# Kernel optimization log

Measured on AMD Instinct MI355X. Metric: run time of the kernel, lower is better.

Reference implementation:

```python
import jax, jax.numpy as jnp
import numpy as np

NUM_TASKS = 5
POOL = 5
R = 8
TOPK = 3
SCALE = 1.0  # module self.scale and forward scale arg, both 1
B, S, DIN, DOUT = 4, 4096, 1024, 1024


def setup_inputs() -> dict:
    key = jax.random.key(0)
    ks = jax.random.split(key, 5)
    inp = {
        "input": jax.random.normal(ks[0], (B, S, DIN), dtype=jnp.float32),
        "W": jax.random.normal(ks[1], (DOUT, DIN), dtype=jnp.float32) / np.sqrt(DIN),
        "lora_down": jax.random.normal(ks[2], (POOL, DIN, R), dtype=jnp.float32) / np.sqrt(DIN),
        "lora_up": jax.random.normal(ks[3], (POOL, R, DOUT), dtype=jnp.float32) / np.sqrt(R),
        "lora_route": jax.random.normal(ks[4], (NUM_TASKS, DIN, POOL), dtype=jnp.float32) * 0.02,
        "task_id": 4,
    }
    return inp


def reference(input, W, lora_down, lora_up, lora_route, task_id):
    # Eval branch (self.training == False), 1 <= task_id <= num_tasks.
    task_id = min(task_id, NUM_TASKS)
    k = min(task_id, TOPK)
    route = lora_route[1]                          # [DIN, POOL] (detach split is a no-op for fwd)
    input_mean = jnp.mean(input, axis=1)           # [B, DIN]
    lora_omegas = jnp.mean(input_mean @ route, axis=0)  # [POOL]
    sliced = lora_omegas[1:task_id + 1]            # source slices from 1
    G, I = jax.lax.top_k(sliced, k)                # indices used DIRECTLY (as in source)
    gate = jax.nn.softmax(G)                       # [k]
    # detached expert products (eval path detaches lora_down @ lora_up)
    dw = jax.lax.stop_gradient(
        jnp.einsum('kdr,kro->kdo', lora_down[I], lora_up[I]))  # [k, DIN, DOUT]
    # delta = sum_i gate[i] * SCALE * (input @ dw[i]); forward scale arg = 1
    delta = SCALE * jnp.einsum('k,bsd,kdo->bso', gate, input, dw)
    # delta_w_all[:B//2] = 0
    bmask = (jnp.arange(input.shape[0]) >= input.shape[0] // 2).astype(delta.dtype)
    delta = delta * bmask[:, None, None]
    return input @ W.T + delta
```

## Files before the change

### kernel.cpp

```cpp
#include <hip/hip_runtime.h>
#include <hip/hip_bf16.h>

typedef __attribute__((ext_vector_type(8))) __bf16 bf16x8;
typedef __attribute__((ext_vector_type(4))) __bf16 bf16x4;
typedef __attribute__((ext_vector_type(4))) float f32x4;

#define DIN 1024
#define DOUT 1024
#define BB 4
#define SS 4096
#define MROWS (BB*SS)
#define POOLN 5
#define RR 8
#define NTASKS 5
#define TOPKK 3

__global__ __launch_bounds__(256) void kA_colsum(const float* __restrict__ in,
                                                 float* __restrict__ partial) {
    const int t = threadIdx.x;
    const int b = blockIdx.x;
    const int tid = b * 256 + t;
    const f32x4* __restrict__ inv = (const f32x4*)in;

    float s0 = 0.f, s1 = 0.f, s2 = 0.f, s3 = 0.f;
    size_t ia = (size_t)tid;
    size_t ib = (size_t)tid + 2097152;
    f32x4 ca = inv[ia];
    f32x4 cb = inv[ib];
#pragma unroll
    for (int i = 0; i < 4; ++i) {
        f32x4 na = ca, nb = cb;
        if (i < 3) {
            na = inv[ia + 524288];
            nb = inv[ib + 524288];
        }
        s0 += ca[0] + cb[0]; s1 += ca[1] + cb[1];
        s2 += ca[2] + cb[2]; s3 += ca[3] + cb[3];
        ca = na; cb = nb;
        ia += 524288; ib += 524288;
    }
    const int c0 = (t * 4) & (DIN - 1);
    f32x4 p = { s0, s1, s2, s3 };
    *(f32x4*)&partial[(size_t)b * DIN + c0] = p;
}

__global__ __launch_bounds__(256) void k1b_reduce(const float* __restrict__ partial,
                                                  float* __restrict__ partial2) {
    const int tid = blockIdx.x * 256 + threadIdx.x;
    const int c = tid & (DIN - 1);
    const int g = tid >> 10;
    float s = 0.f;
    const int r0 = g * 256;
#pragma unroll 8
    for (int r = r0; r < r0 + 256; ++r)
        s += partial[(size_t)r * DIN + c];
    partial2[(size_t)g * DIN + c] = s;
}

__global__ __launch_bounds__(256) void k23_weights(const float* __restrict__ partial2,
                                                   const float* __restrict__ lroute,
                                                   const int* __restrict__ task_id_p,
                                                   const float* __restrict__ W,
                                                   const float* __restrict__ ldown,
                                                   const float* __restrict__ lup,
                                                   __bf16* __restrict__ Wb0,
                                                   __bf16* __restrict__ Wb1) {
    __shared__ float red[4][POOLN];
    __shared__ float sgate[TOPKK];
    __shared__ int   sgidx[TOPKK];
    const int tix = threadIdx.x;
    const int w = tix >> 6, l = tix & 63;

    float part[POOLN] = {0.f, 0.f, 0.f, 0.f, 0.f};
    {
        const int d0 = tix * 4;
#pragma unroll
        for (int dd = 0; dd < 4; ++dd) {
            const int d = d0 + dd;
            float cs = 0.f;
#pragma unroll
            for (int g = 0; g < 8; ++g) cs += partial2[g * DIN + d];
            cs *= (1.0f / (float)MROWS);
            const float* rp = &lroute[(size_t)1 * DIN * POOLN + (size_t)d * POOLN];
#pragma unroll
            for (int p = 0; p < POOLN; ++p) part[p] += cs * rp[p];
        }
    }
#pragma unroll
    for (int p = 0; p < POOLN; ++p) {
        float v = part[p];
        for (int off = 32; off; off >>= 1) v += __shfl_down(v, off);
        if (l == 0) red[w][p] = v;
    }
    __syncthreads();
    if (tix == 0) {
#pragma unroll
        for (int p = 0; p < POOLN; ++p)
            part[p] = red[0][p] + red[1][p] + red[2][p] + red[3][p];
        int tid = *task_id_p;
        if (tid > NTASKS) tid = NTASKS;
        int L = tid < (POOLN - 1) ? tid : (POOLN - 1);
        int k = tid < TOPKK ? tid : TOPKK;
        float sl[POOLN];
        for (int j = 0; j < L; ++j) sl[j] = part[1 + j];
        float G[TOPKK]; int I[TOPKK];
        int used = 0;
        for (int j = 0; j < k; ++j) {
            int best = -1; float bv = 0.f;
            for (int i2 = 0; i2 < L; ++i2) {
                if (used & (1 << i2)) continue;
                if (best < 0 || sl[i2] > bv) { bv = sl[i2]; best = i2; }
            }
            used |= 1 << best; G[j] = bv; I[j] = best;
        }
        float gt[TOPKK] = {0.f, 0.f, 0.f};
        int   gi[TOPKK] = {0, 0, 0};
        if (k > 0) {
            float m = G[0];
            float e[TOPKK]; float se = 0.f;
            for (int j = 0; j < k; ++j) { e[j] = expf(G[j] - m); se += e[j]; }
            for (int j = 0; j < k; ++j) { gt[j] = e[j] / se; gi[j] = I[j]; }
        }
#pragma unroll
        for (int j = 0; j < TOPKK; ++j) { sgate[j] = gt[j]; sgidx[j] = gi[j]; }
    }
    __syncthreads();

    const int o = blockIdx.x;
    const int t = tix;
    float c[TOPKK][RR];
#pragma unroll
    for (int j = 0; j < TOPKK; ++j) {
        const float g = sgate[j];
        const int   p = sgidx[j];
#pragma unroll
        for (int r = 0; r < RR; ++r)
            c[j][r] = g * lup[(size_t)p * RR * DOUT + (size_t)r * DOUT + o];
    }
    const int d0 = t * 4;
    const float4 wv = *(const float4*)&W[(size_t)o * DIN + d0];
    float outv[4] = { wv.x, wv.y, wv.z, wv.w };
    float dwv[4]  = { 0.f, 0.f, 0.f, 0.f };
#pragma unroll
    for (int j = 0; j < TOPKK; ++j) {
        const int p = sgidx[j];
#pragma unroll
        for (int dd = 0; dd < 4; ++dd) {
            const float4 da = *(const float4*)&ldown[(size_t)p * DIN * RR + (size_t)(d0 + dd) * RR];
            const float4 db = *(const float4*)&ldown[(size_t)p * DIN * RR + (size_t)(d0 + dd) * RR + 4];
            dwv[dd] += da.x * c[j][0] + da.y * c[j][1] + da.z * c[j][2] + da.w * c[j][3]
                     + db.x * c[j][4] + db.y * c[j][5] + db.z * c[j][6] + db.w * c[j][7];
        }
    }
    bf16x4 b0 = { (__bf16)outv[0], (__bf16)outv[1], (__bf16)outv[2], (__bf16)outv[3] };
    bf16x4 b1 = { (__bf16)(outv[0] + dwv[0]), (__bf16)(outv[1] + dwv[1]),
                  (__bf16)(outv[2] + dwv[2]), (__bf16)(outv[3] + dwv[3]) };
    *(bf16x4*)&Wb0[(size_t)o * DIN + d0] = b0;
    *(bf16x4*)&Wb1[(size_t)o * DIN + d0] = b1;
}

__global__ __launch_bounds__(512, 4) void k4_gemm(const float* __restrict__ A,
                                                  const __bf16* __restrict__ B0,
                                                  const __bf16* __restrict__ B1,
                                                  float* __restrict__ C) {
    __shared__ ushort lds[36864];
    const int bid = blockIdx.x;
    const int xcd = bid & 7;
    const int idx = bid >> 3;
    const int tm  = xcd * 16 + (idx >> 2);
    const int tn  = idx & 3;
    const __bf16* __restrict__ Bt = (tm >= 64) ? B1 : B0;

    const int tix  = threadIdx.x;
    const int lane = tix & 63;
    const int wid  = tix >> 6;
    const int wm = wid >> 2, wn = wid & 3;

    const int ar = tix >> 2;
    const int ac = tix & 3;
    const f32x4* __restrict__ pA = (const f32x4*)(A + ((size_t)(tm * 128 + ar)) * 1024 + ac * 8);
    const int awrp  = tix >> 3;
    const int awslot= ((tix & 3) + 4 * ((tix >> 2) & 1)) ^ (awrp & 7);
    const int awoff = awrp * 64 + awslot * 8;

    const int rpl  = lane >> 3;
    const int sl   = (lane & 7) ^ rpl;
    const int srow = rpl * 2 + (sl >> 2);
    const int sc   = sl & 3;
    const char* gB = (const char*)Bt + ((size_t)(tn*256 + wid*32 + srow)) * 2048 + sc * 16;
    const int ldsBst = 4096 + wid * 1024;

    const int rhalf = (lane & 15) >> 1;
    const int slot  = ((lane >> 4) + 4 * (lane & 1)) ^ rhalf;
    const int aoff  = (wm * 32 + rhalf) * 64 + slot * 8;
    const int boff  = 4096 + (wn * 32 + rhalf) * 64 + slot * 8;

    f32x4 acc[4][4];
#pragma unroll
    for (int i = 0; i < 4; ++i)
#pragma unroll
        for (int j = 0; j < 4; ++j) acc[i][j] = (f32x4){0.f, 0.f, 0.f, 0.f};

    auto issueB = [&](int s) {
        const int p = s % 3;
        const size_t kb = (size_t)s * 64;
#pragma unroll
        for (int j = 0; j < 2; ++j) {
            __builtin_amdgcn_global_load_lds(
                (const __attribute__((address_space(1))) void*)(gB + (size_t)j * 32768 + kb),
                (__attribute__((address_space(3))) void*)&lds[p * 12288 + ldsBst + j * 512],
                16, 0, 0);
        }
    };

    auto writeA = [&](int s, f32x4 a0, f32x4 a1) {
        const int p = s % 3;
        bf16x8 v = { (__bf16)a0[0], (__bf16)a0[1], (__bf16)a0[2], (__bf16)a0[3],
                     (__bf16)a1[0], (__bf16)a1[1], (__bf16)a1[2], (__bf16)a1[3] };
        *(bf16x8*)&lds[p * 12288 + awoff] = v;
    };

    auto computeSlab = [&](int s) {
        const int p = s % 3;
        const ushort* aB = &lds[p * 12288 + aoff];
        const ushort* bB = &lds[p * 12288 + boff];
        bf16x8 a[4], b[4];
#pragma unroll
        for (int mi = 0; mi < 4; ++mi) a[mi] = *(const bf16x8*)(aB + mi * 512);
#pragma unroll
        for (int ni = 0; ni < 4; ++ni) b[ni] = *(const bf16x8*)(bB + ni * 512);
        __builtin_amdgcn_s_setprio(1);
#pragma unroll
        for (int mi = 0; mi < 4; ++mi)
#pragma unroll
            for (int ni = 0; ni < 4; ++ni)
                acc[mi][ni] = __builtin_amdgcn_mfma_f32_16x16x32_bf16(
                    a[mi], b[ni], acc[mi][ni], 0, 0, 0);
        __builtin_amdgcn_s_setprio(0);
    };

    f32x4 pa0 = pA[0], pa1 = pA[1];
    issueB(0);
    f32x4 na0 = pA[8], na1 = pA[9];
    issueB(1);
    asm volatile("s_waitcnt vmcnt(6)" ::: "memory");
    writeA(0, pa0, pa1);
    asm volatile("s_waitcnt lgkmcnt(0)" ::: "memory");

#pragma unroll 1
    for (int s = 0; s < 32; ++s) {
        if (s < 31) {
            asm volatile("s_waitcnt vmcnt(2)" ::: "memory");
            writeA(s + 1, na0, na1);
        } else {
            asm volatile("s_waitcnt vmcnt(0)" ::: "memory");
        }
        if (s < 30) {
            na0 = pA[(size_t)(s + 2) * 8];
            na1 = pA[(size_t)(s + 2) * 8 + 1];
            issueB(s + 2);
        }
        __builtin_amdgcn_s_barrier();
        asm volatile("" ::: "memory");
        computeSlab(s);
        asm volatile("" ::: "memory");
        asm volatile("s_waitcnt lgkmcnt(0)" ::: "memory");
        __builtin_amdgcn_s_barrier();
    }

#pragma unroll
    for (int mi = 0; mi < 4; ++mi) {
#pragma unroll
        for (int r = 0; r < 4; ++r) {
            const int grow = tm * 128 + wm * 64 + mi * 16 + (lane >> 4) * 4 + r;
            float* cp = C + (size_t)grow * 1024 + tn * 256 + wn * 64 + (lane & 15);
#pragma unroll
            for (int ni = 0; ni < 4; ++ni) cp[ni * 16] = acc[mi][ni][r];
        }
    }
}

extern "C" void kernel_launch(void* const* d_in, const int* in_sizes, int n_in,
                              void* d_out, int out_size, void* d_ws, size_t ws_size,
                              hipStream_t stream) {
    const float* in     = (const float*)d_in[0];
    const float* W      = (const float*)d_in[1];
    const float* ldown  = (const float*)d_in[2];
    const float* lup    = (const float*)d_in[3];
    const float* lroute = (const float*)d_in[4];
    const int*   taskid = (const int*)d_in[5];
    float* out = (float*)d_out;

    __bf16* Wb0     = (__bf16*)d_ws;
    __bf16* Wb1     = Wb0 + (size_t)DOUT * DIN;
    float*  partial2= (float*)(Wb1 + (size_t)DOUT * DIN);
    float*  partial = partial2 + 8 * DIN + 64;

    kA_colsum<<<2048, 256, 0, stream>>>(in, partial);
    k1b_reduce<<<32, 256, 0, stream>>>(partial, partial2);
    k23_weights<<<1024, 256, 0, stream>>>(partial2, lroute, taskid, W, ldown, lup, Wb0, Wb1);
    k4_gemm<<<512, 512, 0, stream>>>(in, Wb0, Wb1, out);
}
```

Baseline: 94.83 us.

## Fuse colsum, reduce and weight-prep kernels into one grid-synced front kernel

Three preliminary kernels (column-sum partials, partial reduction, routing plus merged weight build) become one 512-block kernel. Each block first reduces its input slice and projects it onto the routing matrix, so only 5 floats per block are written instead of a 1024-wide partial row. The blocks then meet at a flag-based grid barrier before every block computes top-k and builds two output rows. This removes two kernel launches and the large partial buffers, at the cost of a memset launch and a spin-wait that needs all 512 blocks to be resident at once.

```diff
diff --git a/kernel.cpp b/kernel.cpp
--- a/kernel.cpp
+++ b/kernel.cpp
@@ -7,156 +7,153 @@
 
 #define DIN 1024
 #define DOUT 1024
-#define BB 4
-#define SS 4096
-#define MROWS (BB*SS)
+#define MROWS 16384
 #define POOLN 5
 #define RR 8
 #define NTASKS 5
 #define TOPKK 3
 
-__global__ __launch_bounds__(256) void kA_colsum(const float* __restrict__ in,
-                                                 float* __restrict__ partial) {
-    const int t = threadIdx.x;
-    const int b = blockIdx.x;
-    const int tid = b * 256 + t;
-    const f32x4* __restrict__ inv = (const f32x4*)in;
-
-    float s0 = 0.f, s1 = 0.f, s2 = 0.f, s3 = 0.f;
-    size_t ia = (size_t)tid;
-    size_t ib = (size_t)tid + 2097152;
-    f32x4 ca = inv[ia];
-    f32x4 cb = inv[ib];
-#pragma unroll
-    for (int i = 0; i < 4; ++i) {
-        f32x4 na = ca, nb = cb;
-        if (i < 3) {
-            na = inv[ia + 524288];
-            nb = inv[ib + 524288];
-        }
-        s0 += ca[0] + cb[0]; s1 += ca[1] + cb[1];
-        s2 += ca[2] + cb[2]; s3 += ca[3] + cb[3];
-        ca = na; cb = nb;
-        ia += 524288; ib += 524288;
-    }
-    const int c0 = (t * 4) & (DIN - 1);
-    f32x4 p = { s0, s1, s2, s3 };
-    *(f32x4*)&partial[(size_t)b * DIN + c0] = p;
-}
-
-__global__ __launch_bounds__(256) void k1b_reduce(const float* __restrict__ partial,
-                                                  float* __restrict__ partial2) {
-    const int tid = blockIdx.x * 256 + threadIdx.x;
-    const int c = tid & (DIN - 1);
-    const int g = tid >> 10;
-    float s = 0.f;
-    const int r0 = g * 256;
-#pragma unroll 8
-    for (int r = r0; r < r0 + 256; ++r)
-        s += partial[(size_t)r * DIN + c];
-    partial2[(size_t)g * DIN + c] = s;
-}
-
-__global__ __launch_bounds__(256) void k23_weights(const float* __restrict__ partial2,
-                                                   const float* __restrict__ lroute,
-                                                   const int* __restrict__ task_id_p,
-                                                   const float* __restrict__ W,
-                                                   const float* __restrict__ ldown,
-                                                   const float* __restrict__ lup,
-                                                   __bf16* __restrict__ Wb0,
-                                                   __bf16* __restrict__ Wb1) {
+__global__ __launch_bounds__(256, 4) void kFront(
+        const float* __restrict__ in, const float* __restrict__ W,
+        const float* __restrict__ ldown, const float* __restrict__ lup,
+        const float* __restrict__ lroute, const int* __restrict__ task_id_p,
+        __bf16* __restrict__ Wb0, __bf16* __restrict__ Wb1,
+        float* __restrict__ omgpart, unsigned* __restrict__ flags) {
     __shared__ float red[4][POOLN];
     __shared__ float sgate[TOPKK];
     __shared__ int   sgidx[TOPKK];
-    const int tix = threadIdx.x;
-    const int w = tix >> 6, l = tix & 63;
-
-    float part[POOLN] = {0.f, 0.f, 0.f, 0.f, 0.f};
+    const int b = blockIdx.x;
+    const int t = threadIdx.x;
+    const int w = t >> 6, l = t & 63;
+
+    const f32x4* __restrict__ inv = (const f32x4*)in;
+    float s0 = 0.f, s1 = 0.f, s2 = 0.f, s3 = 0.f;
+    size_t ia = (size_t)b * 32 * 256 + t;
+    size_t ib = ia + 16 * 256;
+    f32x4 ca = inv[ia], cb = inv[ib];
+#pragma unroll
+    for (int i = 0; i < 16; ++i) {
+        f32x4 na = ca, nb = cb;
+        if (i < 15) { na = inv[ia + 256]; nb = inv[ib + 256]; }
+        s0 += ca[0] + cb[0]; s1 += ca[1] + cb[1];
+        s2 += ca[2] + cb[2]; s3 += ca[3] + cb[3];
+        ca = na; cb = nb; ia += 256; ib += 256;
+    }
+
+    float om[POOLN];
     {
-        const int d0 = tix * 4;
-#pragma unroll
-        for (int dd = 0; dd < 4; ++dd) {
-            const int d = d0 + dd;
-            float cs = 0.f;
-#pragma unroll
-            for (int g = 0; g < 8; ++g) cs += partial2[g * DIN + d];
-            cs *= (1.0f / (float)MROWS);
-            const float* rp = &lroute[(size_t)1 * DIN * POOLN + (size_t)d * POOLN];
-#pragma unroll
-            for (int p = 0; p < POOLN; ++p) part[p] += cs * rp[p];
-        }
+        const float* rp = &lroute[(size_t)DIN * POOLN + (size_t)(4 * t) * POOLN];
+        const float sj[4] = { s0, s1, s2, s3 };
+#pragma unroll
+        for (int p = 0; p < POOLN; ++p) om[p] = 0.f;
+#pragma unroll
+        for (int j = 0; j < 4; ++j)
+#pragma unroll
+            for (int p = 0; p < POOLN; ++p)
+                om[p] += sj[j] * rp[j * POOLN + p];
     }
 #pragma unroll
     for (int p = 0; p < POOLN; ++p) {
-        float v = part[p];
+        float v = om[p];
         for (int off = 32; off; off >>= 1) v += __shfl_down(v, off);
         if (l == 0) red[w][p] = v;
     }
     __syncthreads();
-    if (tix == 0) {
+    if (t == 0) {
 #pragma unroll
         for (int p = 0; p < POOLN; ++p)
-            part[p] = red[0][p] + red[1][p] + red[2][p] + red[3][p];
-        int tid = *task_id_p;
-        if (tid > NTASKS) tid = NTASKS;
-        int L = tid < (POOLN - 1) ? tid : (POOLN - 1);
-        int k = tid < TOPKK ? tid : TOPKK;
-        float sl[POOLN];
-        for (int j = 0; j < L; ++j) sl[j] = part[1 + j];
-        float G[TOPKK]; int I[TOPKK];
-        int used = 0;
-        for (int j = 0; j < k; ++j) {
-            int best = -1; float bv = 0.f;
-            for (int i2 = 0; i2 < L; ++i2) {
-                if (used & (1 << i2)) continue;
-                if (best < 0 || sl[i2] > bv) { bv = sl[i2]; best = i2; }
+            omgpart[b * 8 + p] = red[0][p] + red[1][p] + red[2][p] + red[3][p];
+        __threadfence();
+        __hip_atomic_store(&flags[b], 1u, __ATOMIC_RELEASE, __HIP_MEMORY_SCOPE_AGENT);
+    }
+
+    while (__hip_atomic_load(&flags[t], __ATOMIC_RELAXED, __HIP_MEMORY_SCOPE_AGENT) == 0u)
+        __builtin_amdgcn_s_sleep(8);
+    while (__hip_atomic_load(&flags[t + 256], __ATOMIC_RELAXED, __HIP_MEMORY_SCOPE_AGENT) == 0u)
+        __builtin_amdgcn_s_sleep(8);
+    __syncthreads();
+    __threadfence();
+
+    {
+        float acc[POOLN];
+#pragma unroll
+        for (int p = 0; p < POOLN; ++p)
+            acc[p] = omgpart[t * 8 + p] + omgpart[(t + 256) * 8 + p];
+#pragma unroll
+        for (int p = 0; p < POOLN; ++p) {
+            float v = acc[p];
+            for (int off = 32; off; off >>= 1) v += __shfl_down(v, off);
+            if (l == 0) red[w][p] = v;
+        }
+        __syncthreads();
+        if (t == 0) {
+            float part[POOLN];
+#pragma unroll
+            for (int p = 0; p < POOLN; ++p)
+                part[p] = (red[0][p] + red[1][p] + red[2][p] + red[3][p]) * (1.0f / (float)MROWS);
+            int tid = *task_id_p;
+            if (tid > NTASKS) tid = NTASKS;
+            int L = tid < (POOLN - 1) ? tid : (POOLN - 1);
+            int k = tid < TOPKK ? tid : TOPKK;
+            float sl[POOLN];
+            for (int j = 0; j < L; ++j) sl[j] = part[1 + j];
+            float G[TOPKK]; int I[TOPKK];
+            int used = 0;
+            for (int j = 0; j < k; ++j) {
+                int best = -1; float bv = 0.f;
+                for (int i2 = 0; i2 < L; ++i2) {
+                    if (used & (1 << i2)) continue;
+                    if (best < 0 || sl[i2] > bv) { bv = sl[i2]; best = i2; }
+                }
+                used |= 1 << best; G[j] = bv; I[j] = best;
             }
-            used |= 1 << best; G[j] = bv; I[j] = best;
-        }
-        float gt[TOPKK] = {0.f, 0.f, 0.f};
-        int   gi[TOPKK] = {0, 0, 0};
-        if (k > 0) {
-            float m = G[0];
-            float e[TOPKK]; float se = 0.f;
-            for (int j = 0; j < k; ++j) { e[j] = expf(G[j] - m); se += e[j]; }
-            for (int j = 0; j < k; ++j) { gt[j] = e[j] / se; gi[j] = I[j]; }
-        }
-#pragma unroll
-        for (int j = 0; j < TOPKK; ++j) { sgate[j] = gt[j]; sgidx[j] = gi[j]; }
-    }
-    __syncthreads();
-
-    const int o = blockIdx.x;
-    const int t = tix;
-    float c[TOPKK][RR];
-#pragma unroll
-    for (int j = 0; j < TOPKK; ++j) {
-        const float g = sgate[j];
-        const int   p = sgidx[j];
-#pragma unroll
-        for (int r = 0; r < RR; ++r)
-            c[j][r] = g * lup[(size_t)p * RR * DOUT + (size_t)r * DOUT + o];
-    }
-    const int d0 = t * 4;
-    const float4 wv = *(const float4*)&W[(size_t)o * DIN + d0];
-    float outv[4] = { wv.x, wv.y, wv.z, wv.w };
-    float dwv[4]  = { 0.f, 0.f, 0.f, 0.f };
-#pragma unroll
-    for (int j = 0; j < TOPKK; ++j) {
-        const int p = sgidx[j];
-#pragma unroll
-        for (int dd = 0; dd < 4; ++dd) {
-            const float4 da = *(const float4*)&ldown[(size_t)p * DIN * RR + (size_t)(d0 + dd) * RR];
-            const float4 db = *(const float4*)&ldown[(size_t)p * DIN * RR + (size_t)(d0 + dd) * RR + 4];
-            dwv[dd] += da.x * c[j][0] + da.y * c[j][1] + da.z * c[j][2] + da.w * c[j][3]
-                     + db.x * c[j][4] + db.y * c[j][5] + db.z * c[j][6] + db.w * c[j][7];
-        }
-    }
-    bf16x4 b0 = { (__bf16)outv[0], (__bf16)outv[1], (__bf16)outv[2], (__bf16)outv[3] };
-    bf16x4 b1 = { (__bf16)(outv[0] + dwv[0]), (__bf16)(outv[1] + dwv[1]),
-                  (__bf16)(outv[2] + dwv[2]), (__bf16)(outv[3] + dwv[3]) };
-    *(bf16x4*)&Wb0[(size_t)o * DIN + d0] = b0;
-    *(bf16x4*)&Wb1[(size_t)o * DIN + d0] = b1;
+            float gt[TOPKK] = {0.f, 0.f, 0.f};
+            int   gi[TOPKK] = {0, 0, 0};
+            if (k > 0) {
+                float m = G[0];
+                float e[TOPKK]; float se = 0.f;
+                for (int j = 0; j < k; ++j) { e[j] = expf(G[j] - m); se += e[j]; }
+                for (int j = 0; j < k; ++j) { gt[j] = e[j] / se; gi[j] = I[j]; }
+            }
+#pragma unroll
+            for (int j = 0; j < TOPKK; ++j) { sgate[j] = gt[j]; sgidx[j] = gi[j]; }
+        }
+        __syncthreads();
+    }
+
+#pragma unroll
+    for (int rep = 0; rep < 2; ++rep) {
+        const int o = b * 2 + rep;
+        float c[TOPKK][RR];
+#pragma unroll
+        for (int j = 0; j < TOPKK; ++j) {
+            const float g = sgate[j];
+            const int   p = sgidx[j];
+#pragma unroll
+            for (int r = 0; r < RR; ++r)
+                c[j][r] = g * lup[(size_t)p * RR * DOUT + (size_t)r * DOUT + o];
+        }
+        const int d0 = t * 4;
+        const float4 wv = *(const float4*)&W[(size_t)o * DIN + d0];
+        float outv[4] = { wv.x, wv.y, wv.z, wv.w };
+        float dwv[4]  = { 0.f, 0.f, 0.f, 0.f };
+#pragma unroll
+        for (int j = 0; j < TOPKK; ++j) {
+            const int p = sgidx[j];
+#pragma unroll
+            for (int dd = 0; dd < 4; ++dd) {
+                const float4 da = *(const float4*)&ldown[(size_t)p * DIN * RR + (size_t)(d0 + dd) * RR];
+                const float4 db = *(const float4*)&ldown[(size_t)p * DIN * RR + (size_t)(d0 + dd) * RR + 4];
+                dwv[dd] += da.x * c[j][0] + da.y * c[j][1] + da.z * c[j][2] + da.w * c[j][3]
+                         + db.x * c[j][4] + db.y * c[j][5] + db.z * c[j][6] + db.w * c[j][7];
+            }
+        }
+        bf16x4 b0 = { (__bf16)outv[0], (__bf16)outv[1], (__bf16)outv[2], (__bf16)outv[3] };
+        bf16x4 b1 = { (__bf16)(outv[0] + dwv[0]), (__bf16)(outv[1] + dwv[1]),
+                      (__bf16)(outv[2] + dwv[2]), (__bf16)(outv[3] + dwv[3]) };
+        *(bf16x4*)&Wb0[(size_t)o * DIN + d0] = b0;
+        *(bf16x4*)&Wb1[(size_t)o * DIN + d0] = b1;
+    }
 }
 
 __global__ __launch_bounds__(512, 4) void k4_gemm(const float* __restrict__ A,
@@ -291,13 +288,13 @@
     const int*   taskid = (const int*)d_in[5];
     float* out = (float*)d_out;
 
-    __bf16* Wb0     = (__bf16*)d_ws;
-    __bf16* Wb1     = Wb0 + (size_t)DOUT * DIN;
-    float*  partial2= (float*)(Wb1 + (size_t)DOUT * DIN);
-    float*  partial = partial2 + 8 * DIN + 64;
-
-    kA_colsum<<<2048, 256, 0, stream>>>(in, partial);
-    k1b_reduce<<<32, 256, 0, stream>>>(partial, partial2);
-    k23_weights<<<1024, 256, 0, stream>>>(partial2, lroute, taskid, W, ldown, lup, Wb0, Wb1);
+    __bf16*   Wb0     = (__bf16*)d_ws;
+    __bf16*   Wb1     = Wb0 + (size_t)DOUT * DIN;
+    float*    omgpart = (float*)(Wb1 + (size_t)DOUT * DIN);
+    unsigned* flags   = (unsigned*)(omgpart + 512 * 8);
+
+    hipMemsetAsync(flags, 0, 512 * sizeof(unsigned), stream);
+    kFront<<<512, 256, 0, stream>>>(in, W, ldown, lup, lroute, taskid,
+                                    Wb0, Wb1, omgpart, flags);
     k4_gemm<<<512, 512, 0, stream>>>(in, Wb0, Wb1, out);
 }
```

After: 127.6 us. 34.5% more time.

## Overlap first-half GEMM with column-sum reduction in a mixed kernel

Applied to the files above, without the earlier changes.

Splits the GEMM so the batch half that needs only plain W (bf16 converted by a new small kernel) runs in the same launch as the input column-sum blocks. The route-dependent corrected weight is then built and the second half GEMM runs separately. The aim is to hide the input-mean reduction and weight prep behind useful GEMM work instead of serialising them before the whole GEMM. In exchange it adds a launch and splits the GEMM into two 256-block launches, which may underfill the GPU and leave tails.

```diff
diff --git a/kernel.cpp b/kernel.cpp
--- a/kernel.cpp
+++ b/kernel.cpp
@@ -7,41 +7,172 @@
 
 #define DIN 1024
 #define DOUT 1024
-#define BB 4
-#define SS 4096
-#define MROWS (BB*SS)
+#define MROWS 16384
 #define POOLN 5
 #define RR 8
 #define NTASKS 5
 #define TOPKK 3
 
-__global__ __launch_bounds__(256) void kA_colsum(const float* __restrict__ in,
+__device__ __forceinline__ void gemm_tile(const float* __restrict__ A,
+                                          const __bf16* __restrict__ Bt,
+                                          float* __restrict__ C,
+                                          int tm, int tn, int tix,
+                                          ushort* lds) {
+    const int lane = tix & 63;
+    const int wid  = tix >> 6;
+    const int wm = wid >> 2, wn = wid & 3;
+
+    const int ar = tix >> 2;
+    const int ac = tix & 3;
+    const f32x4* __restrict__ pA = (const f32x4*)(A + ((size_t)(tm * 128 + ar)) * 1024 + ac * 8);
+    const int awrp  = tix >> 3;
+    const int awslot= ((tix & 3) + 4 * ((tix >> 2) & 1)) ^ (awrp & 7);
+    const int awoff = awrp * 64 + awslot * 8;
+
+    const int rpl  = lane >> 3;
+    const int sl   = (lane & 7) ^ rpl;
+    const int srow = rpl * 2 + (sl >> 2);
+    const int sc   = sl & 3;
+    const char* gB = (const char*)Bt + ((size_t)(tn*256 + wid*32 + srow)) * 2048 + sc * 16;
+    const int ldsBst = 4096 + wid * 1024;
+
+    const int rhalf = (lane & 15) >> 1;
+    const int slot  = ((lane >> 4) + 4 * (lane & 1)) ^ rhalf;
+    const int aoff  = (wm * 32 + rhalf) * 64 + slot * 8;
+    const int boff  = 4096 + (wn * 32 + rhalf) * 64 + slot * 8;
+
+    f32x4 acc[4][4];
+#pragma unroll
+    for (int i = 0; i < 4; ++i)
+#pragma unroll
+        for (int j = 0; j < 4; ++j) acc[i][j] = (f32x4){0.f, 0.f, 0.f, 0.f};
+
+    auto issueB = [&](int s) {
+        const int p = s % 3;
+        const size_t kb = (size_t)s * 64;
+#pragma unroll
+        for (int j = 0; j < 2; ++j) {
+            __builtin_amdgcn_global_load_lds(
+                (const __attribute__((address_space(1))) void*)(gB + (size_t)j * 32768 + kb),
+                (__attribute__((address_space(3))) void*)&lds[p * 12288 + ldsBst + j * 512],
+                16, 0, 0);
+        }
+    };
+
+    auto writeA = [&](int s, f32x4 a0, f32x4 a1) {
+        const int p = s % 3;
+        bf16x8 v = { (__bf16)a0[0], (__bf16)a0[1], (__bf16)a0[2], (__bf16)a0[3],
+                     (__bf16)a1[0], (__bf16)a1[1], (__bf16)a1[2], (__bf16)a1[3] };
+        *(bf16x8*)&lds[p * 12288 + awoff] = v;
+    };
+
+    auto computeSlab = [&](int s) {
+        const int p = s % 3;
+        const ushort* aB = &lds[p * 12288 + aoff];
+        const ushort* bB = &lds[p * 12288 + boff];
+        bf16x8 a[4], b[4];
+#pragma unroll
+        for (int mi = 0; mi < 4; ++mi) a[mi] = *(const bf16x8*)(aB + mi * 512);
+#pragma unroll
+        for (int ni = 0; ni < 4; ++ni) b[ni] = *(const bf16x8*)(bB + ni * 512);
+        __builtin_amdgcn_s_setprio(1);
+#pragma unroll
+        for (int mi = 0; mi < 4; ++mi)
+#pragma unroll
+            for (int ni = 0; ni < 4; ++ni)
+                acc[mi][ni] = __builtin_amdgcn_mfma_f32_16x16x32_bf16(
+                    a[mi], b[ni], acc[mi][ni], 0, 0, 0);
+        __builtin_amdgcn_s_setprio(0);
+    };
+
+    f32x4 pa0 = pA[0], pa1 = pA[1];
+    issueB(0);
+    f32x4 na0 = pA[8], na1 = pA[9];
+    issueB(1);
+    asm volatile("s_waitcnt vmcnt(6)" ::: "memory");
+    writeA(0, pa0, pa1);
+    asm volatile("s_waitcnt lgkmcnt(0)" ::: "memory");
+
+#pragma unroll 1
+    for (int s = 0; s < 32; ++s) {
+        if (s < 31) {
+            asm volatile("s_waitcnt vmcnt(2)" ::: "memory");
+            writeA(s + 1, na0, na1);
+        } else {
+            asm volatile("s_waitcnt vmcnt(0)" ::: "memory");
+        }
+        if (s < 30) {
+            na0 = pA[(size_t)(s + 2) * 8];
+            na1 = pA[(size_t)(s + 2) * 8 + 1];
+            issueB(s + 2);
+        }
+        __builtin_amdgcn_s_barrier();
+        asm volatile("" ::: "memory");
+        computeSlab(s);
+        asm volatile("" ::: "memory");
+        asm volatile("s_waitcnt lgkmcnt(0)" ::: "memory");
+        __builtin_amdgcn_s_barrier();
+    }
+
+#pragma unroll
+    for (int mi = 0; mi < 4; ++mi) {
+#pragma unroll
+        for (int r = 0; r < 4; ++r) {
+            const int grow = tm * 128 + wm * 64 + mi * 16 + (lane >> 4) * 4 + r;
+            float* cp = C + (size_t)grow * 1024 + tn * 256 + wn * 64 + (lane & 15);
+#pragma unroll
+            for (int ni = 0; ni < 4; ++ni) cp[ni * 16] = acc[mi][ni][r];
+        }
+    }
+}
+
+__global__ __launch_bounds__(256) void kW_cvt(const float* __restrict__ W,
+                                              __bf16* __restrict__ Wb0) {
+    const size_t i = (size_t)(blockIdx.x * 256 + threadIdx.x) * 8;
+    f32x4 a = *(const f32x4*)&W[i];
+    f32x4 b = *(const f32x4*)&W[i + 4];
+    bf16x8 v = { (__bf16)a[0], (__bf16)a[1], (__bf16)a[2], (__bf16)a[3],
+                 (__bf16)b[0], (__bf16)b[1], (__bf16)b[2], (__bf16)b[3] };
+    *(bf16x8*)&Wb0[i] = v;
+}
+
+__global__ __launch_bounds__(512, 4) void k1_mix(const float* __restrict__ in,
+                                                 const __bf16* __restrict__ Wb0,
+                                                 float* __restrict__ C,
                                                  float* __restrict__ partial) {
-    const int t = threadIdx.x;
-    const int b = blockIdx.x;
-    const int tid = b * 256 + t;
-    const f32x4* __restrict__ inv = (const f32x4*)in;
-
+    __shared__ ushort lds[36864];
+    const int bid = blockIdx.x;
+    if (bid < 256) {
+        const int xcd = bid & 7;
+        const int idx = bid >> 3;
+        gemm_tile(in, Wb0, C, xcd * 8 + (idx >> 2), idx & 3, threadIdx.x, lds);
+        return;
+    }
+    const int cb = bid - 256;
+    const int t  = threadIdx.x;
+    const int cq = t & 255;
+    const int h  = t >> 8;
+    const f32x4* __restrict__ base = (const f32x4*)in
+        + ((size_t)(cb * 256 + h * 128)) * 256 + cq;
     float s0 = 0.f, s1 = 0.f, s2 = 0.f, s3 = 0.f;
-    size_t ia = (size_t)tid;
-    size_t ib = (size_t)tid + 2097152;
-    f32x4 ca = inv[ia];
-    f32x4 cb = inv[ib];
-#pragma unroll
-    for (int i = 0; i < 4; ++i) {
-        f32x4 na = ca, nb = cb;
-        if (i < 3) {
-            na = inv[ia + 524288];
-            nb = inv[ib + 524288];
-        }
-        s0 += ca[0] + cb[0]; s1 += ca[1] + cb[1];
-        s2 += ca[2] + cb[2]; s3 += ca[3] + cb[3];
-        ca = na; cb = nb;
-        ia += 524288; ib += 524288;
-    }
-    const int c0 = (t * 4) & (DIN - 1);
-    f32x4 p = { s0, s1, s2, s3 };
-    *(f32x4*)&partial[(size_t)b * DIN + c0] = p;
+#pragma unroll 1
+    for (int j = 0; j < 16; ++j) {
+        const f32x4* p = base + (size_t)j * 8 * 256;
+        f32x4 v0 = p[0];
+        f32x4 v1 = p[256];
+        f32x4 v2 = p[512];
+        f32x4 v3 = p[768];
+        f32x4 v4 = p[1024];
+        f32x4 v5 = p[1280];
+        f32x4 v6 = p[1536];
+        f32x4 v7 = p[1792];
+        s0 += v0[0] + v1[0] + v2[0] + v3[0] + v4[0] + v5[0] + v6[0] + v7[0];
+        s1 += v0[1] + v1[1] + v2[1] + v3[1] + v4[1] + v5[1] + v6[1] + v7[1];
+        s2 += v0[2] + v1[2] + v2[2] + v3[2] + v4[2] + v5[2] + v6[2] + v7[2];
+        s3 += v0[3] + v1[3] + v2[3] + v3[3] + v4[3] + v5[3] + v6[3] + v7[3];
+    }
+    f32x4 pv = { s0, s1, s2, s3 };
+    *(f32x4*)&partial[(size_t)(cb * 2 + h) * DIN + cq * 4] = pv;
 }
 
 __global__ __launch_bounds__(256) void k1b_reduce(const float* __restrict__ partial,
@@ -50,21 +181,20 @@
     const int c = tid & (DIN - 1);
     const int g = tid >> 10;
     float s = 0.f;
-    const int r0 = g * 256;
+    const int r0 = g * 16;
 #pragma unroll 8
-    for (int r = r0; r < r0 + 256; ++r)
+    for (int r = r0; r < r0 + 16; ++r)
         s += partial[(size_t)r * DIN + c];
     partial2[(size_t)g * DIN + c] = s;
 }
 
-__global__ __launch_bounds__(256) void k23_weights(const float* __restrict__ partial2,
-                                                   const float* __restrict__ lroute,
-                                                   const int* __restrict__ task_id_p,
-                                                   const float* __restrict__ W,
-                                                   const float* __restrict__ ldown,
-                                                   const float* __restrict__ lup,
-                                                   __bf16* __restrict__ Wb0,
-                                                   __bf16* __restrict__ Wb1) {
+__global__ __launch_bounds__(256) void k23b_weights(const float* __restrict__ partial2,
+                                                    const float* __restrict__ lroute,
+                                                    const int* __restrict__ task_id_p,
+                                                    const float* __restrict__ W,
+                                                    const float* __restrict__ ldown,
+                                                    const float* __restrict__ lup,
+                                                    __bf16* __restrict__ Wb1) {
     __shared__ float red[4][POOLN];
     __shared__ float sgate[TOPKK];
     __shared__ int   sgidx[TOPKK];
@@ -127,7 +257,6 @@
     __syncthreads();
 
     const int o = blockIdx.x;
-    const int t = tix;
     float c[TOPKK][RR];
 #pragma unroll
     for (int j = 0; j < TOPKK; ++j) {
@@ -137,10 +266,9 @@
         for (int r = 0; r < RR; ++r)
             c[j][r] = g * lup[(size_t)p * RR * DOUT + (size_t)r * DOUT + o];
     }
-    const int d0 = t * 4;
+    const int d0 = tix * 4;
     const float4 wv = *(const float4*)&W[(size_t)o * DIN + d0];
-    float outv[4] = { wv.x, wv.y, wv.z, wv.w };
-    float dwv[4]  = { 0.f, 0.f, 0.f, 0.f };
+    float dwv[4] = { 0.f, 0.f, 0.f, 0.f };
 #pragma unroll
     for (int j = 0; j < TOPKK; ++j) {
         const int p = sgidx[j];
@@ -152,132 +280,19 @@
                      + db.x * c[j][4] + db.y * c[j][5] + db.z * c[j][6] + db.w * c[j][7];
         }
     }
-    bf16x4 b0 = { (__bf16)outv[0], (__bf16)outv[1], (__bf16)outv[2], (__bf16)outv[3] };
-    bf16x4 b1 = { (__bf16)(outv[0] + dwv[0]), (__bf16)(outv[1] + dwv[1]),
-                  (__bf16)(outv[2] + dwv[2]), (__bf16)(outv[3] + dwv[3]) };
-    *(bf16x4*)&Wb0[(size_t)o * DIN + d0] = b0;
+    bf16x4 b1 = { (__bf16)(wv.x + dwv[0]), (__bf16)(wv.y + dwv[1]),
+                  (__bf16)(wv.z + dwv[2]), (__bf16)(wv.w + dwv[3]) };
     *(bf16x4*)&Wb1[(size_t)o * DIN + d0] = b1;
 }
 
-__global__ __launch_bounds__(512, 4) void k4_gemm(const float* __restrict__ A,
-                                                  const __bf16* __restrict__ B0,
-                                                  const __bf16* __restrict__ B1,
+__global__ __launch_bounds__(512, 4) void k3_gemm(const float* __restrict__ in,
+                                                  const __bf16* __restrict__ Wb1,
                                                   float* __restrict__ C) {
     __shared__ ushort lds[36864];
     const int bid = blockIdx.x;
     const int xcd = bid & 7;
     const int idx = bid >> 3;
-    const int tm  = xcd * 16 + (idx >> 2);
-    const int tn  = idx & 3;
-    const __bf16* __restrict__ Bt = (tm >= 64) ? B1 : B0;
-
-    const int tix  = threadIdx.x;
-    const int lane = tix & 63;
-    const int wid  = tix >> 6;
-    const int wm = wid >> 2, wn = wid & 3;
-
-    const int ar = tix >> 2;
-    const int ac = tix & 3;
-    const f32x4* __restrict__ pA = (const f32x4*)(A + ((size_t)(tm * 128 + ar)) * 1024 + ac * 8);
-    const int awrp  = tix >> 3;
-    const int awslot= ((tix & 3) + 4 * ((tix >> 2) & 1)) ^ (awrp & 7);
-    const int awoff = awrp * 64 + awslot * 8;
-
-    const int rpl  = lane >> 3;
-    const int sl   = (lane & 7) ^ rpl;
-    const int srow = rpl * 2 + (sl >> 2);
-    const int sc   = sl & 3;
-    const char* gB = (const char*)Bt + ((size_t)(tn*256 + wid*32 + srow)) * 2048 + sc * 16;
-    const int ldsBst = 4096 + wid * 1024;
-
-    const int rhalf = (lane & 15) >> 1;
-    const int slot  = ((lane >> 4) + 4 * (lane & 1)) ^ rhalf;
-    const int aoff  = (wm * 32 + rhalf) * 64 + slot * 8;
-    const int boff  = 4096 + (wn * 32 + rhalf) * 64 + slot * 8;
-
-    f32x4 acc[4][4];
-#pragma unroll
-    for (int i = 0; i < 4; ++i)
-#pragma unroll
-        for (int j = 0; j < 4; ++j) acc[i][j] = (f32x4){0.f, 0.f, 0.f, 0.f};
-
-    auto issueB = [&](int s) {
-        const int p = s % 3;
-        const size_t kb = (size_t)s * 64;
-#pragma unroll
-        for (int j = 0; j < 2; ++j) {
-            __builtin_amdgcn_global_load_lds(
-                (const __attribute__((address_space(1))) void*)(gB + (size_t)j * 32768 + kb),
-                (__attribute__((address_space(3))) void*)&lds[p * 12288 + ldsBst + j * 512],
-                16, 0, 0);
-        }
-    };
-
-    auto writeA = [&](int s, f32x4 a0, f32x4 a1) {
-        const int p = s % 3;
-        bf16x8 v = { (__bf16)a0[0], (__bf16)a0[1], (__bf16)a0[2], (__bf16)a0[3],
-                     (__bf16)a1[0], (__bf16)a1[1], (__bf16)a1[2], (__bf16)a1[3] };
-        *(bf16x8*)&lds[p * 12288 + awoff] = v;
-    };
-
-    auto computeSlab = [&](int s) {
-        const int p = s % 3;
-        const ushort* aB = &lds[p * 12288 + aoff];
-        const ushort* bB = &lds[p * 12288 + boff];
-        bf16x8 a[4], b[4];
-#pragma unroll
-        for (int mi = 0; mi < 4; ++mi) a[mi] = *(const bf16x8*)(aB + mi * 512);
-#pragma unroll
-        for (int ni = 0; ni < 4; ++ni) b[ni] = *(const bf16x8*)(bB + ni * 512);
-        __builtin_amdgcn_s_setprio(1);
-#pragma unroll
-        for (int mi = 0; mi < 4; ++mi)
-#pragma unroll
-            for (int ni = 0; ni < 4; ++ni)
-                acc[mi][ni] = __builtin_amdgcn_mfma_f32_16x16x32_bf16(
-                    a[mi], b[ni], acc[mi][ni], 0, 0, 0);
-        __builtin_amdgcn_s_setprio(0);
-    };
-
-    f32x4 pa0 = pA[0], pa1 = pA[1];
-    issueB(0);
-    f32x4 na0 = pA[8], na1 = pA[9];
-    issueB(1);
-    asm volatile("s_waitcnt vmcnt(6)" ::: "memory");
-    writeA(0, pa0, pa1);
-    asm volatile("s_waitcnt lgkmcnt(0)" ::: "memory");
-
-#pragma unroll 1
-    for (int s = 0; s < 32; ++s) {
-        if (s < 31) {
-            asm volatile("s_waitcnt vmcnt(2)" ::: "memory");
-            writeA(s + 1, na0, na1);
-        } else {
-            asm volatile("s_waitcnt vmcnt(0)" ::: "memory");
-        }
-        if (s < 30) {
-            na0 = pA[(size_t)(s + 2) * 8];
-            na1 = pA[(size_t)(s + 2) * 8 + 1];
-            issueB(s + 2);
-        }
-        __builtin_amdgcn_s_barrier();
-        asm volatile("" ::: "memory");
-        computeSlab(s);
-        asm volatile("" ::: "memory");
-        asm volatile("s_waitcnt lgkmcnt(0)" ::: "memory");
-        __builtin_amdgcn_s_barrier();
-    }
-
-#pragma unroll
-    for (int mi = 0; mi < 4; ++mi) {
-#pragma unroll
-        for (int r = 0; r < 4; ++r) {
-            const int grow = tm * 128 + wm * 64 + mi * 16 + (lane >> 4) * 4 + r;
-            float* cp = C + (size_t)grow * 1024 + tn * 256 + wn * 64 + (lane & 15);
-#pragma unroll
-            for (int ni = 0; ni < 4; ++ni) cp[ni * 16] = acc[mi][ni][r];
-        }
-    }
+    gemm_tile(in, Wb1, C, 64 + xcd * 8 + (idx >> 2), idx & 3, threadIdx.x, lds);
 }
 
 extern "C" void kernel_launch(void* const* d_in, const int* in_sizes, int n_in,
@@ -291,13 +306,14 @@
     const int*   taskid = (const int*)d_in[5];
     float* out = (float*)d_out;
 
-    __bf16* Wb0     = (__bf16*)d_ws;
-    __bf16* Wb1     = Wb0 + (size_t)DOUT * DIN;
-    float*  partial2= (float*)(Wb1 + (size_t)DOUT * DIN);
-    float*  partial = partial2 + 8 * DIN + 64;
-
-    kA_colsum<<<2048, 256, 0, stream>>>(in, partial);
+    __bf16* Wb0      = (__bf16*)d_ws;
+    __bf16* Wb1      = Wb0 + (size_t)DOUT * DIN;
+    float*  partial  = (float*)(Wb1 + (size_t)DOUT * DIN);
+    float*  partial2 = partial + 128 * DIN;
+
+    kW_cvt<<<512, 256, 0, stream>>>(W, Wb0);
+    k1_mix<<<320, 512, 0, stream>>>(in, Wb0, out, partial);
     k1b_reduce<<<32, 256, 0, stream>>>(partial, partial2);
-    k23_weights<<<1024, 256, 0, stream>>>(partial2, lroute, taskid, W, ldown, lup, Wb0, Wb1);
-    k4_gemm<<<512, 512, 0, stream>>>(in, Wb0, Wb1, out);
-}
+    k23b_weights<<<1024, 256, 0, stream>>>(partial2, lroute, taskid, W, ldown, lup, Wb1);
+    k3_gemm<<<256, 512, 0, stream>>>(in, Wb1, out);
+}
```

Result: faster. 90.81 us (-4.2%).
